# Performance work log

Hardware: AMD Instinct MI355X
Metric: run time of the kernel (lower is better)

The kernel has to match this reference:

```python
import jax, jax.numpy as jnp
import numpy as np

NUM_NEIGHBORS = 10
BN_EPS = 1e-5


def setup_inputs() -> dict:
    key = jax.random.key(0)
    ks = jax.random.split(key, 6)
    B, N, D = 8, 4096, 64
    x = jax.random.normal(ks[0], (B, N, D), jnp.float32)

    def w(k, shape):
        return jax.random.normal(k, shape, jnp.float32) * 0.05

    return {
        "x": x,
        "gamma": jnp.ones((D,), jnp.float32),
        "beta": jnp.zeros((D,), jnp.float32),
        "W1": w(ks[1], (128, 128)), "b1": jnp.zeros((128,), jnp.float32),
        "W2": w(ks[2], (128, 64)), "b2": jnp.zeros((64,), jnp.float32),
        "W3": w(ks[3], (64, 64)), "b3": jnp.zeros((64,), jnp.float32),
        "Wg": w(ks[4], (128, 64)), "bg": jnp.zeros((64,), jnp.float32),
    }


def reference(x, gamma, beta, W1, b1, W2, b2, W3, b3, Wg, bg):
    B, N, D = x.shape
    K = NUM_NEIGHBORS

    # BatchNorm1d in train mode: normalize over all B*N rows with batch stats
    xf = x.reshape(-1, D)
    mu = jnp.mean(xf, axis=0)
    var = jnp.mean((xf - mu) ** 2, axis=0)  # biased, as torch BN uses
    xn = (((xf - mu) / jnp.sqrt(var + BN_EPS)) * gamma + beta).reshape(B, N, D)

    # KNN in feature space (standard DGCNN gather_neighbours)
    sq = jnp.sum(xn * xn, axis=-1)  # [B,N]
    dist = sq[:, :, None] + sq[:, None, :] - 2.0 * jnp.einsum("bnd,bmd->bnm", xn, xn)
    _, idx = jax.lax.top_k(-dist, K)  # [B,N,K] indices of nearest (incl. self)

    # gather neighbor features: neigh[b,n,k,:] = xn[b, idx[b,n,k], :]
    neigh = jax.vmap(lambda f, i: f[i])(xn, idx)  # [B,N,K,D]

    exp = jnp.broadcast_to(xn[:, :, None, :], (B, N, K, D))
    edge = jnp.concatenate([exp, exp - neigh], axis=-1)  # [B,N,K,2D]

    h = jax.nn.relu(edge @ W1 + b1)
    h = jax.nn.relu(h @ W2 + b2)
    h = jax.nn.relu(h @ W3 + b3)  # [B,N,K,64]

    vert = jnp.max(h, axis=2)  # max over neighbors -> [B,N,64]
    g = jnp.max(vert, axis=1, keepdims=True)  # global max-pool [B,1,64]
    cat = jnp.concatenate([vert, jnp.broadcast_to(g, vert.shape)], axis=-1)  # [B,N,128]
    return jax.nn.relu(cat @ Wg + bg)  # [B,N,64]
```

## Files before the change

### kernel.cpp

```cpp
#include <hip/hip_runtime.h>
#include <hip/hip_fp16.h>
#include <float.h>

#define BB 8
#define NN 4096
#define DD 64
#define KNBR 10
#define ROWS (BB*NN)

typedef _Float16 f16x8 __attribute__((ext_vector_type(8)));
typedef float f32x4 __attribute__((ext_vector_type(4)));

__global__ void k_bn_stats(const float* __restrict__ x, float* __restrict__ stats) {
  __shared__ float ls[2][4][64];
  int d = threadIdx.x & 63;
  int g = threadIdx.x >> 6;
  float s = 0.f, s2 = 0.f;
  for (int r = blockIdx.x * 4 + g; r < ROWS; r += gridDim.x * 4) {
    float val = x[r * 64 + d];
    s += val;
    s2 = fmaf(val, val, s2);
  }
  ls[0][g][d] = s;
  ls[1][g][d] = s2;
  __syncthreads();
  if (g == 0) {
    atomicAdd(&stats[d],      ls[0][0][d] + ls[0][1][d] + ls[0][2][d] + ls[0][3][d]);
    atomicAdd(&stats[64 + d], ls[1][0][d] + ls[1][1][d] + ls[1][2][d] + ls[1][3][d]);
  }
}

__global__ void k_bn_finalize(const float* __restrict__ stats,
                              const float* __restrict__ gamma,
                              const float* __restrict__ beta,
                              float* __restrict__ ss) {
  int d = threadIdx.x;
  const float inv = 1.f / 32768.f;
  float mu  = stats[d] * inv;
  float var = stats[64 + d] * inv - mu * mu;
  float sc  = gamma[d] / sqrtf(var + 1e-5f);
  ss[d]      = sc;
  ss[64 + d] = beta[d] - mu * sc;
}

__global__ void k_normalize(const float* __restrict__ x, const float* __restrict__ ss,
                            float* __restrict__ xn, float* __restrict__ sq,
                            _Float16* __restrict__ xh, _Float16* __restrict__ xl) {
  int row = blockIdx.x * 4 + (threadIdx.x >> 6);
  int d = threadIdx.x & 63;
  int idx = row * 64 + d;
  float val = fmaf(x[idx], ss[d], ss[64 + d]);
  xn[idx] = val;
  _Float16 h = (_Float16)val;
  _Float16 l = (_Float16)(val - (float)h);
  xh[idx] = h;
  xl[idx] = l;
  float p = val * val;
  #pragma unroll
  for (int off = 32; off > 0; off >>= 1) p += __shfl_xor(p, off);
  if (d == 0) sq[row] = p;
}

__global__ __launch_bounds__(512, 2) void k_knn(const _Float16* __restrict__ xh,
                                                const _Float16* __restrict__ xl,
                                                const float* __restrict__ sq,
                                                int* __restrict__ knn) {
  __shared__ __align__(16) float Dws[8][2112];
  __shared__ float thrs[64];
  __shared__ int cnts[64];
  const int tid = threadIdx.x;
  const int w = tid >> 6, lane = tid & 63;
  const int l15 = lane & 15, lg = lane >> 4;
  const int b = blockIdx.x >> 6;
  const int rowbase = (blockIdx.x & 63) << 6;
  const int bN = b * NN;
  const _Float16* __restrict__ xhb = xh + (size_t)bN * 64;
  const _Float16* __restrict__ xlb = xl + (size_t)bN * 64;
  const float* __restrict__ sqb = sq + bN;

  f16x8 Ah[4][2], Al[4][2];
  #pragma unroll
  for (int mt = 0; mt < 4; ++mt) {
    #pragma unroll
    for (int ks = 0; ks < 2; ++ks) {
      int r = rowbase + mt * 16 + l15;
      Ah[mt][ks] = *(const f16x8*)(xhb + r * 64 + ks * 32 + lg * 8);
      Al[mt][ks] = *(const f16x8*)(xlb + r * 64 + ks * 32 + lg * 8);
    }
  }

  float bd[10];
  #pragma unroll
  for (int i = 0; i < 10; ++i) bd[i] = FLT_MAX;

  float* Dw = Dws[w];
  float* Drow = Dw + lane * 33;
  const int mbase0 = w * 512;

  #pragma unroll 1
  for (int t = 0; t < 16; ++t) {
    const int mb = mbase0 + t * 32;
    #pragma unroll
    for (int s = 0; s < 2; ++s) {
      const int ms = mb + s * 16;
      f16x8 Bh[2], Bl[2];
      #pragma unroll
      for (int ks = 0; ks < 2; ++ks) {
        Bh[ks] = *(const f16x8*)(xhb + (ms + l15) * 64 + ks * 32 + lg * 8);
        Bl[ks] = *(const f16x8*)(xlb + (ms + l15) * 64 + ks * 32 + lg * 8);
      }
      float sqv = sqb[ms + l15];
      #pragma unroll
      for (int mt = 0; mt < 4; ++mt) {
        f32x4 a = {0.f, 0.f, 0.f, 0.f};
        #pragma unroll
        for (int ks = 0; ks < 2; ++ks) {
          a = __builtin_amdgcn_mfma_f32_16x16x32_f16(Ah[mt][ks], Bh[ks], a, 0, 0, 0);
          a = __builtin_amdgcn_mfma_f32_16x16x32_f16(Ah[mt][ks], Bl[ks], a, 0, 0, 0);
          a = __builtin_amdgcn_mfma_f32_16x16x32_f16(Al[mt][ks], Bh[ks], a, 0, 0, 0);
        }
        int rw = mt * 16 + lg * 4;
        #pragma unroll
        for (int r2 = 0; r2 < 4; ++r2)
          Dw[(rw + r2) * 33 + s * 16 + l15] = fmaf(-2.f, a[r2], sqv);
      }
    }
    #pragma unroll 4
    for (int mm = 0; mm < 32; ++mm) {
      float cd = Drow[mm];
      if (cd < bd[9]) {
        float prev = bd[0];
        bd[0] = fminf(cd, bd[0]);
        #pragma unroll
        for (int j = 1; j < 10; ++j) {
          float cur = bd[j];
          bd[j] = fminf(cur, fmaxf(prev, cd));
          prev = cur;
        }
      }
    }
  }

  __syncthreads();
  float* md = &Dws[0][0];
  #pragma unroll
  for (int i = 0; i < 10; ++i) md[(w * 64 + lane) * 10 + i] = bd[i];
  if (tid < 64) cnts[tid] = 0;
  __syncthreads();
  if (tid < 64) {
    float fd[10];
    #pragma unroll
    for (int i = 0; i < 10; ++i) fd[i] = FLT_MAX;
    for (int li = 0; li < 8; ++li) {
      #pragma unroll 1
      for (int kk = 0; kk < 10; ++kk) {
        float cd = md[(li * 64 + tid) * 10 + kk];
        if (cd < fd[9]) {
          float prev = fd[0];
          fd[0] = fminf(cd, fd[0]);
          #pragma unroll
          for (int j = 1; j < 10; ++j) {
            float cur = fd[j];
            fd[j] = fminf(cur, fmaxf(prev, cd));
            prev = cur;
          }
        } else break;
      }
    }
    thrs[tid] = fd[9];
  }
  __syncthreads();

  float thv[4][4];
  #pragma unroll
  for (int mt = 0; mt < 4; ++mt)
    #pragma unroll
    for (int r2 = 0; r2 < 4; ++r2)
      thv[mt][r2] = thrs[mt * 16 + lg * 4 + r2];
  int* knnrow = knn + (size_t)(bN + rowbase) * KNBR;

  #pragma unroll 1
  for (int t = 0; t < 16; ++t) {
    const int mb = mbase0 + t * 32;
    #pragma unroll
    for (int s = 0; s < 2; ++s) {
      const int ms = mb + s * 16;
      f16x8 Bh[2], Bl[2];
      #pragma unroll
      for (int ks = 0; ks < 2; ++ks) {
        Bh[ks] = *(const f16x8*)(xhb + (ms + l15) * 64 + ks * 32 + lg * 8);
        Bl[ks] = *(const f16x8*)(xlb + (ms + l15) * 64 + ks * 32 + lg * 8);
      }
      float sqv = sqb[ms + l15];
      #pragma unroll
      for (int mt = 0; mt < 4; ++mt) {
        f32x4 a = {0.f, 0.f, 0.f, 0.f};
        #pragma unroll
        for (int ks = 0; ks < 2; ++ks) {
          a = __builtin_amdgcn_mfma_f32_16x16x32_f16(Ah[mt][ks], Bh[ks], a, 0, 0, 0);
          a = __builtin_amdgcn_mfma_f32_16x16x32_f16(Ah[mt][ks], Bl[ks], a, 0, 0, 0);
          a = __builtin_amdgcn_mfma_f32_16x16x32_f16(Al[mt][ks], Bh[ks], a, 0, 0, 0);
        }
        #pragma unroll
        for (int r2 = 0; r2 < 4; ++r2) {
          float cd = fmaf(-2.f, a[r2], sqv);
          if (cd <= thv[mt][r2]) {
            int row = mt * 16 + lg * 4 + r2;
            int slot = atomicAdd(&cnts[row], 1);
            if (slot < KNBR) knnrow[row * KNBR + slot] = bN + ms + l15;
          }
        }
      }
    }
  }
}

__global__ void k_uv(const float* __restrict__ xn, const float* __restrict__ W1,
                     const float* __restrict__ b1, float* __restrict__ u,
                     float* __restrict__ v) {
  __shared__ float xs[64 * 64];
  const int tid = threadIdx.x;
  const int o = tid & 127;
  const bool isU = tid < 128;
  const int rowbase = blockIdx.x * 64;

  float wreg[64];
  #pragma unroll
  for (int d = 0; d < 64; ++d) {
    float bw = W1[(64 + d) * 128 + o];
    wreg[d] = isU ? (W1[d * 128 + o] + bw) : bw;
  }
  const float bb = isU ? b1[o] : 0.f;
  float* __restrict__ dst = isU ? u : v;

  {
    const float4* s4 = (const float4*)(xn + rowbase * 64);
    float4* d4 = (float4*)xs;
    #pragma unroll
    for (int i = 0; i < 4; ++i) d4[tid + 256 * i] = s4[tid + 256 * i];
  }
  __syncthreads();

  for (int r = 0; r < 64; ++r) {
    const float4* xr = (const float4*)(xs + r * 64);
    float a0 = bb, a1 = 0.f, a2 = 0.f, a3 = 0.f;
    #pragma unroll
    for (int q = 0; q < 16; ++q) {
      float4 xv = xr[q];
      a0 = fmaf(xv.x, wreg[4 * q + 0], a0);
      a1 = fmaf(xv.y, wreg[4 * q + 1], a1);
      a2 = fmaf(xv.z, wreg[4 * q + 2], a2);
      a3 = fmaf(xv.w, wreg[4 * q + 3], a3);
    }
    dst[(rowbase + r) * 128 + o] = (a0 + a1) + (a2 + a3);
  }
}

__global__ __launch_bounds__(256, 2) void k_edge(const float* __restrict__ uu,
                                                 const float* __restrict__ vv,
                                                 const int* __restrict__ knn,
                                                 const float* __restrict__ W2,
                                                 const float* __restrict__ b2,
                                                 const float* __restrict__ W3,
                                                 const float* __restrict__ b3,
                                                 float* __restrict__ vert) {
  __shared__ __align__(16) _Float16 W3Ts[64 * 72];
  __shared__ __align__(16) _Float16 h2buf[4][16 * 88];
  __shared__ int vmaxs[4][512];
  const int tid = threadIdx.x;
  const int w = tid >> 6, lane = tid & 63;
  const int l15 = lane & 15, lg = lane >> 4;

  for (int i = tid; i < 64 * 64; i += 256) {
    int o3 = i >> 6, k2 = i & 63;
    W3Ts[o3 * 72 + k2] = (_Float16)W3[k2 * 64 + o3];
  }
  f16x8 w2f[4][4];
  #pragma unroll
  for (int ks = 0; ks < 4; ++ks) {
    #pragma unroll
    for (int nt = 0; nt < 4; ++nt) {
      f16x8 t;
      #pragma unroll
      for (int j = 0; j < 8; ++j)
        t[j] = (_Float16)W2[(ks * 32 + lg * 8 + j) * 64 + nt * 16 + l15];
      w2f[ks][nt] = t;
    }
  }
  float bias2[4], bias3[4];
  #pragma unroll
  for (int nt = 0; nt < 4; ++nt) { bias2[nt] = b2[nt * 16 + l15]; bias3[nt] = b3[nt * 16 + l15]; }

  _Float16* h2w = h2buf[w];
  int* vmaxw = vmaxs[w];
  #pragma unroll
  for (int q = 0; q < 8; ++q) vmaxw[lane * 8 + q] = 0;
  __syncthreads();

  const int g = blockIdx.x * 4 + w;
  const int n0 = g * 8;
  const int ebase = n0 * KNBR;
  #pragma unroll 1
  for (int mt = 0; mt < 5; ++mt) {
    const int e = mt * 16 + l15;
    const int m = knn[ebase + e];
    const int n = n0 + e / 10;
    const float* Up = uu + (size_t)n * 128 + lg * 8;
    const float* Vp = vv + (size_t)m * 128 + lg * 8;
    f16x8 A[4];
    #pragma unroll
    for (int ks = 0; ks < 4; ++ks) {
      float4 ua = *(const float4*)(Up + ks * 32);
      float4 ub = *(const float4*)(Up + ks * 32 + 4);
      float4 va = *(const float4*)(Vp + ks * 32);
      float4 vb = *(const float4*)(Vp + ks * 32 + 4);
      f16x8 t;
      t[0] = (_Float16)fmaxf(ua.x - va.x, 0.f);
      t[1] = (_Float16)fmaxf(ua.y - va.y, 0.f);
      t[2] = (_Float16)fmaxf(ua.z - va.z, 0.f);
      t[3] = (_Float16)fmaxf(ua.w - va.w, 0.f);
      t[4] = (_Float16)fmaxf(ub.x - vb.x, 0.f);
      t[5] = (_Float16)fmaxf(ub.y - vb.y, 0.f);
      t[6] = (_Float16)fmaxf(ub.z - vb.z, 0.f);
      t[7] = (_Float16)fmaxf(ub.w - vb.w, 0.f);
      A[ks] = t;
    }
    f32x4 acc[4];
    #pragma unroll
    for (int nt = 0; nt < 4; ++nt) { float bbv = bias2[nt]; acc[nt] = (f32x4){bbv, bbv, bbv, bbv}; }
    #pragma unroll
    for (int ks = 0; ks < 4; ++ks) {
      #pragma unroll
      for (int nt = 0; nt < 4; ++nt)
        acc[nt] = __builtin_amdgcn_mfma_f32_16x16x32_f16(A[ks], w2f[ks][nt], acc[nt], 0, 0, 0);
    }
    #pragma unroll
    for (int nt = 0; nt < 4; ++nt) {
      #pragma unroll
      for (int r = 0; r < 4; ++r)
        h2w[(lg * 4 + r) * 88 + nt * 16 + l15] = (_Float16)fmaxf(acc[nt][r], 0.f);
    }
    f16x8 A3[2];
    #pragma unroll
    for (int ks2 = 0; ks2 < 2; ++ks2)
      A3[ks2] = *(const f16x8*)(h2w + l15 * 88 + ks2 * 32 + lg * 8);
    f32x4 c3[4];
    #pragma unroll
    for (int nt = 0; nt < 4; ++nt) { float bbv = bias3[nt]; c3[nt] = (f32x4){bbv, bbv, bbv, bbv}; }
    #pragma unroll
    for (int ks2 = 0; ks2 < 2; ++ks2) {
      #pragma unroll
      for (int nt = 0; nt < 4; ++nt) {
        f16x8 bf = *(const f16x8*)(W3Ts + (nt * 16 + l15) * 72 + ks2 * 32 + lg * 8);
        c3[nt] = __builtin_amdgcn_mfma_f32_16x16x32_f16(A3[ks2], bf, c3[nt], 0, 0, 0);
      }
    }
    #pragma unroll
    for (int nt = 0; nt < 4; ++nt) {
      #pragma unroll
      for (int r = 0; r < 4; ++r) {
        float val = fmaxf(c3[nt][r], 0.f);
        int e2 = mt * 16 + lg * 4 + r;
        int p = e2 / 10;
        atomicMax(&vmaxw[p * 64 + nt * 16 + l15], __float_as_int(val));
      }
    }
  }
  {
    int p2 = lane >> 3, c0 = (lane & 7) * 8;
    const int* vp = &vmaxw[p2 * 64 + c0];
    float4 r0, r1;
    r0.x = __int_as_float(vp[0]); r0.y = __int_as_float(vp[1]);
    r0.z = __int_as_float(vp[2]); r0.w = __int_as_float(vp[3]);
    r1.x = __int_as_float(vp[4]); r1.y = __int_as_float(vp[5]);
    r1.z = __int_as_float(vp[6]); r1.w = __int_as_float(vp[7]);
    *(float4*)(vert + (size_t)(n0 + p2) * 64 + c0) = r0;
    *(float4*)(vert + (size_t)(n0 + p2) * 64 + c0 + 4) = r1;
  }
}

__global__ void k_gmax(const float* __restrict__ vert, float* __restrict__ g) {
  __shared__ float red[4][64];
  int b = blockIdx.x >> 4, chunk = blockIdx.x & 15;
  int sub = threadIdx.x >> 6, o = threadIdx.x & 63;
  float vm = 0.f;
  for (int j = 0; j < 64; ++j) {
    int r = chunk * 256 + j * 4 + sub;
    vm = fmaxf(vm, vert[(b * NN + r) * 64 + o]);
  }
  red[sub][o] = vm;
  __syncthreads();
  if (sub == 0) {
    float mm = fmaxf(fmaxf(red[0][o], red[1][o]), fmaxf(red[2][o], red[3][o]));
    atomicMax((int*)&g[b * 64 + o], __float_as_int(mm));
  }
}

__global__ void k_gb(const float* __restrict__ g, const float* __restrict__ Wg,
                     const float* __restrict__ bg, float* __restrict__ gb) {
  int t = threadIdx.x;
  int b = t >> 6, o = t & 63;
  float acc = bg[o];
  #pragma unroll
  for (int i = 0; i < 64; ++i)
    acc = fmaf(g[b * 64 + i], Wg[(64 + i) * 64 + o], acc);
  gb[b * 64 + o] = acc;
}

__global__ void k_final(const float* __restrict__ vert, const float* __restrict__ Wg,
                        const float* __restrict__ gb, float* __restrict__ out) {
  __shared__ float Wgs[64 * 64];
  int tid = threadIdx.x, w = tid >> 6, lane = tid & 63;
  for (int i = tid; i < 4096; i += 256) Wgs[i] = Wg[i];
  __syncthreads();
  int gw = blockIdx.x * 4 + w;
  for (int j = 0; j < 4; ++j) {
    int n = gw + 8192 * j;
    int b = n >> 12;
    float vrow = vert[n * 64 + lane];
    float ac0 = gb[b * 64 + lane], ac1 = 0.f, ac2 = 0.f, ac3 = 0.f;
    #pragma unroll
    for (int i = 0; i < 64; i += 4) {
      ac0 = fmaf(__shfl(vrow, i),     Wgs[i * 64 + lane],       ac0);
      ac1 = fmaf(__shfl(vrow, i + 1), Wgs[(i + 1) * 64 + lane], ac1);
      ac2 = fmaf(__shfl(vrow, i + 2), Wgs[(i + 2) * 64 + lane], ac2);
      ac3 = fmaf(__shfl(vrow, i + 3), Wgs[(i + 3) * 64 + lane], ac3);
    }
    out[n * 64 + lane] = fmaxf((ac0 + ac1) + (ac2 + ac3), 0.f);
  }
}

extern "C" void kernel_launch(void* const* d_in, const int* in_sizes, int n_in,
                              void* d_out, int out_size, void* d_ws, size_t ws_size,
                              hipStream_t stream) {
  const float* x     = (const float*)d_in[0];
  const float* gamma = (const float*)d_in[1];
  const float* beta  = (const float*)d_in[2];
  const float* W1    = (const float*)d_in[3];
  const float* b1    = (const float*)d_in[4];
  const float* W2    = (const float*)d_in[5];
  const float* b2    = (const float*)d_in[6];
  const float* W3    = (const float*)d_in[7];
  const float* b3    = (const float*)d_in[8];
  const float* Wg    = (const float*)d_in[9];
  const float* bg    = (const float*)d_in[10];
  float* out = (float*)d_out;

  float* ws    = (float*)d_ws;
  float* stats = ws;
  float* ss    = ws + 128;
  float* xn    = ws + 256;
  float* sq    = xn + 2097152;
  int*   knn   = (int*)(sq + 32768);
  float* u     = (float*)(knn + 327680);
  float* v     = u + 4194304;
  float* vert  = v + 4194304;
  float* g     = vert + 2097152;
  float* gb    = g + 512;
  _Float16* xh = (_Float16*)(gb + 512);
  _Float16* xl = (_Float16*)(gb + 512 + 1048576);

  hipMemsetAsync(stats, 0, 128 * sizeof(float), stream);
  hipMemsetAsync(g, 0, 512 * sizeof(float), stream);

  k_bn_stats<<<256, 256, 0, stream>>>(x, stats);
  k_bn_finalize<<<1, 64, 0, stream>>>(stats, gamma, beta, ss);
  k_normalize<<<8192, 256, 0, stream>>>(x, ss, xn, sq, xh, xl);
  k_knn<<<512, 512, 0, stream>>>(xh, xl, sq, knn);
  k_uv<<<512, 256, 0, stream>>>(xn, W1, b1, u, v);
  k_edge<<<1024, 256, 0, stream>>>(u, v, knn, W2, b2, W3, b3, vert);
  k_gmax<<<128, 256, 0, stream>>>(vert, g);
  k_gb<<<1, 512, 0, stream>>>(g, Wg, bg, gb);
  k_final<<<2048, 256, 0, stream>>>(vert, Wg, gb, out);
}
```

Before: 523.1 us.

## Split KNN candidate range across two blocks, stage B tiles in swizzled LDS

The KNN kernel is split so that each query tile is handled by two 256-thread blocks, each scanning half of the candidate points. Each half writes its 10 best (distance, index) pairs, and a new selection kernel merges the 20 candidates per row into the final top-10. Candidate tiles are now prefetched into registers and staged through XOR-swizzled LDS rather than loaded directly from global memory per MFMA. The intent is more blocks and better load latency hiding, at the cost of an extra launch, a scratch buffer aliased onto u, and a second pass over the candidate distances.

```diff
diff --git a/kernel.cpp b/kernel.cpp
--- a/kernel.cpp
+++ b/kernel.cpp
@@ -61,22 +61,30 @@
   if (d == 0) sq[row] = p;
 }
 
-__global__ __launch_bounds__(512, 2) void k_knn(const _Float16* __restrict__ xh,
-                                                const _Float16* __restrict__ xl,
-                                                const float* __restrict__ sq,
-                                                int* __restrict__ knn) {
-  __shared__ __align__(16) float Dws[8][2112];
+__global__ __launch_bounds__(256, 2) void k_knn_ab(const _Float16* __restrict__ xh,
+                                                   const _Float16* __restrict__ xl,
+                                                   const float* __restrict__ sq,
+                                                   float* __restrict__ pairs,
+                                                   int* __restrict__ pidx) {
+  __shared__ __align__(16) char lds[33792];
   __shared__ float thrs[64];
   __shared__ int cnts[64];
   const int tid = threadIdx.x;
   const int w = tid >> 6, lane = tid & 63;
   const int l15 = lane & 15, lg = lane >> 4;
-  const int b = blockIdx.x >> 6;
-  const int rowbase = (blockIdx.x & 63) << 6;
+  const int bid = blockIdx.x;
+  const int h = bid & 1;
+  const int qb = bid >> 1;
+  const int b = qb >> 6;
+  const int rowbase = (qb & 63) << 6;
   const int bN = b * NN;
   const _Float16* __restrict__ xhb = xh + (size_t)bN * 64;
   const _Float16* __restrict__ xlb = xl + (size_t)bN * 64;
-  const float* __restrict__ sqb = sq + bN;
+
+  char* wbase = lds + w * 8448;
+  char* Bhi = wbase;
+  char* Blo = wbase + 2048;
+  float* Dw = (float*)(wbase + 4096);
 
   f16x8 Ah[4][2], Al[4][2];
   #pragma unroll
@@ -93,40 +101,59 @@
   #pragma unroll
   for (int i = 0; i < 10; ++i) bd[i] = FLT_MAX;
 
-  float* Dw = Dws[w];
-  float* Drow = Dw + lane * 33;
-  const int mbase0 = w * 512;
+  int srow[2], scc[2];
+  #pragma unroll
+  for (int i = 0; i < 2; ++i) { int c = i * 64 + lane; srow[i] = c >> 3; scc[i] = c & 7; }
+
+  const int mbase0 = h * 2048 + w * 512;
+  f16x8 sh[2], sl[2];
+  #pragma unroll
+  for (int i = 0; i < 2; ++i) {
+    sh[i] = *(const f16x8*)(xhb + (mbase0 + srow[i]) * 64 + scc[i] * 8);
+    sl[i] = *(const f16x8*)(xlb + (mbase0 + srow[i]) * 64 + scc[i] * 8);
+  }
+
+  float* Drow = Dw + lane * 17;
 
   #pragma unroll 1
-  for (int t = 0; t < 16; ++t) {
-    const int mb = mbase0 + t * 32;
-    #pragma unroll
-    for (int s = 0; s < 2; ++s) {
-      const int ms = mb + s * 16;
-      f16x8 Bh[2], Bl[2];
+  for (int t = 0; t < 32; ++t) {
+    const int mb = mbase0 + t * 16;
+    const int mb2 = (t < 31) ? mb + 16 : mb;
+    float sqv = sq[bN + mb + l15];
+    #pragma unroll
+    for (int i = 0; i < 2; ++i) {
+      int off = srow[i] * 128 + 16 * (scc[i] ^ (srow[i] & 7));
+      *(f16x8*)(Bhi + off) = sh[i];
+      *(f16x8*)(Blo + off) = sl[i];
+    }
+    #pragma unroll
+    for (int i = 0; i < 2; ++i) {
+      sh[i] = *(const f16x8*)(xhb + (mb2 + srow[i]) * 64 + scc[i] * 8);
+      sl[i] = *(const f16x8*)(xlb + (mb2 + srow[i]) * 64 + scc[i] * 8);
+    }
+    f16x8 Bh[2], Bl[2];
+    #pragma unroll
+    for (int ks = 0; ks < 2; ++ks) {
+      int off = l15 * 128 + 16 * ((ks * 4 + lg) ^ (l15 & 7));
+      Bh[ks] = *(const f16x8*)(Bhi + off);
+      Bl[ks] = *(const f16x8*)(Blo + off);
+    }
+    #pragma unroll
+    for (int mt = 0; mt < 4; ++mt) {
+      f32x4 a0 = {0.f, 0.f, 0.f, 0.f};
       #pragma unroll
       for (int ks = 0; ks < 2; ++ks) {
-        Bh[ks] = *(const f16x8*)(xhb + (ms + l15) * 64 + ks * 32 + lg * 8);
-        Bl[ks] = *(const f16x8*)(xlb + (ms + l15) * 64 + ks * 32 + lg * 8);
-      }
-      float sqv = sqb[ms + l15];
-      #pragma unroll
-      for (int mt = 0; mt < 4; ++mt) {
-        f32x4 a = {0.f, 0.f, 0.f, 0.f};
-        #pragma unroll
-        for (int ks = 0; ks < 2; ++ks) {
-          a = __builtin_amdgcn_mfma_f32_16x16x32_f16(Ah[mt][ks], Bh[ks], a, 0, 0, 0);
-          a = __builtin_amdgcn_mfma_f32_16x16x32_f16(Ah[mt][ks], Bl[ks], a, 0, 0, 0);
-          a = __builtin_amdgcn_mfma_f32_16x16x32_f16(Al[mt][ks], Bh[ks], a, 0, 0, 0);
-        }
-        int rw = mt * 16 + lg * 4;
-        #pragma unroll
-        for (int r2 = 0; r2 < 4; ++r2)
-          Dw[(rw + r2) * 33 + s * 16 + l15] = fmaf(-2.f, a[r2], sqv);
-      }
+        a0 = __builtin_amdgcn_mfma_f32_16x16x32_f16(Ah[mt][ks], Bh[ks], a0, 0, 0, 0);
+        a0 = __builtin_amdgcn_mfma_f32_16x16x32_f16(Ah[mt][ks], Bl[ks], a0, 0, 0, 0);
+        a0 = __builtin_amdgcn_mfma_f32_16x16x32_f16(Al[mt][ks], Bh[ks], a0, 0, 0, 0);
+      }
+      int rw = mt * 16 + lg * 4;
+      #pragma unroll
+      for (int r2 = 0; r2 < 4; ++r2)
+        Dw[(rw + r2) * 17 + l15] = fmaf(-2.f, a0[r2], sqv);
     }
     #pragma unroll 4
-    for (int mm = 0; mm < 32; ++mm) {
+    for (int mm = 0; mm < 16; ++mm) {
       float cd = Drow[mm];
       if (cd < bd[9]) {
         float prev = bd[0];
@@ -142,7 +169,7 @@
   }
 
   __syncthreads();
-  float* md = &Dws[0][0];
+  float* md = (float*)lds;
   #pragma unroll
   for (int i = 0; i < 10; ++i) md[(w * 64 + lane) * 10 + i] = bd[i];
   if (tid < 64) cnts[tid] = 0;
@@ -151,10 +178,10 @@
     float fd[10];
     #pragma unroll
     for (int i = 0; i < 10; ++i) fd[i] = FLT_MAX;
-    for (int li = 0; li < 8; ++li) {
+    for (int w2 = 0; w2 < 4; ++w2) {
       #pragma unroll 1
       for (int kk = 0; kk < 10; ++kk) {
-        float cd = md[(li * 64 + tid) * 10 + kk];
+        float cd = md[(w2 * 64 + tid) * 10 + kk];
         if (cd < fd[9]) {
           float prev = fd[0];
           fd[0] = fminf(cd, fd[0]);
@@ -177,42 +204,86 @@
     #pragma unroll
     for (int r2 = 0; r2 < 4; ++r2)
       thv[mt][r2] = thrs[mt * 16 + lg * 4 + r2];
-  int* knnrow = knn + (size_t)(bN + rowbase) * KNBR;
-
+
+  float* prow = pairs + (size_t)(bN + rowbase) * 20 + h * 10;
+  int*   irow = pidx  + (size_t)(bN + rowbase) * 20 + h * 10;
+
+  #pragma unroll
+  for (int i = 0; i < 2; ++i) {
+    sh[i] = *(const f16x8*)(xhb + (mbase0 + srow[i]) * 64 + scc[i] * 8);
+    sl[i] = *(const f16x8*)(xlb + (mbase0 + srow[i]) * 64 + scc[i] * 8);
+  }
   #pragma unroll 1
-  for (int t = 0; t < 16; ++t) {
-    const int mb = mbase0 + t * 32;
-    #pragma unroll
-    for (int s = 0; s < 2; ++s) {
-      const int ms = mb + s * 16;
-      f16x8 Bh[2], Bl[2];
+  for (int t = 0; t < 32; ++t) {
+    const int mb = mbase0 + t * 16;
+    const int mb2 = (t < 31) ? mb + 16 : mb;
+    float sqv = sq[bN + mb + l15];
+    #pragma unroll
+    for (int i = 0; i < 2; ++i) {
+      int off = srow[i] * 128 + 16 * (scc[i] ^ (srow[i] & 7));
+      *(f16x8*)(Bhi + off) = sh[i];
+      *(f16x8*)(Blo + off) = sl[i];
+    }
+    #pragma unroll
+    for (int i = 0; i < 2; ++i) {
+      sh[i] = *(const f16x8*)(xhb + (mb2 + srow[i]) * 64 + scc[i] * 8);
+      sl[i] = *(const f16x8*)(xlb + (mb2 + srow[i]) * 64 + scc[i] * 8);
+    }
+    f16x8 Bh[2], Bl[2];
+    #pragma unroll
+    for (int ks = 0; ks < 2; ++ks) {
+      int off = l15 * 128 + 16 * ((ks * 4 + lg) ^ (l15 & 7));
+      Bh[ks] = *(const f16x8*)(Bhi + off);
+      Bl[ks] = *(const f16x8*)(Blo + off);
+    }
+    #pragma unroll
+    for (int mt = 0; mt < 4; ++mt) {
+      f32x4 a0 = {0.f, 0.f, 0.f, 0.f};
       #pragma unroll
       for (int ks = 0; ks < 2; ++ks) {
-        Bh[ks] = *(const f16x8*)(xhb + (ms + l15) * 64 + ks * 32 + lg * 8);
-        Bl[ks] = *(const f16x8*)(xlb + (ms + l15) * 64 + ks * 32 + lg * 8);
-      }
-      float sqv = sqb[ms + l15];
-      #pragma unroll
-      for (int mt = 0; mt < 4; ++mt) {
-        f32x4 a = {0.f, 0.f, 0.f, 0.f};
-        #pragma unroll
-        for (int ks = 0; ks < 2; ++ks) {
-          a = __builtin_amdgcn_mfma_f32_16x16x32_f16(Ah[mt][ks], Bh[ks], a, 0, 0, 0);
-          a = __builtin_amdgcn_mfma_f32_16x16x32_f16(Ah[mt][ks], Bl[ks], a, 0, 0, 0);
-          a = __builtin_amdgcn_mfma_f32_16x16x32_f16(Al[mt][ks], Bh[ks], a, 0, 0, 0);
-        }
-        #pragma unroll
-        for (int r2 = 0; r2 < 4; ++r2) {
-          float cd = fmaf(-2.f, a[r2], sqv);
-          if (cd <= thv[mt][r2]) {
-            int row = mt * 16 + lg * 4 + r2;
-            int slot = atomicAdd(&cnts[row], 1);
-            if (slot < KNBR) knnrow[row * KNBR + slot] = bN + ms + l15;
+        a0 = __builtin_amdgcn_mfma_f32_16x16x32_f16(Ah[mt][ks], Bh[ks], a0, 0, 0, 0);
+        a0 = __builtin_amdgcn_mfma_f32_16x16x32_f16(Ah[mt][ks], Bl[ks], a0, 0, 0, 0);
+        a0 = __builtin_amdgcn_mfma_f32_16x16x32_f16(Al[mt][ks], Bh[ks], a0, 0, 0, 0);
+      }
+      #pragma unroll
+      for (int r2 = 0; r2 < 4; ++r2) {
+        float d0 = fmaf(-2.f, a0[r2], sqv);
+        int row = mt * 16 + lg * 4 + r2;
+        if (d0 <= thv[mt][r2]) {
+          int slot = atomicAdd(&cnts[row], 1);
+          if (slot < KNBR) {
+            prow[row * 20 + slot] = d0;
+            irow[row * 20 + slot] = bN + mb + l15;
           }
         }
       }
     }
   }
+}
+
+__global__ void k_sel(const float* __restrict__ pairs, const int* __restrict__ pidx,
+                      int* __restrict__ knn) {
+  int gid = blockIdx.x * 256 + threadIdx.x;
+  const float* pd = pairs + (size_t)gid * 20;
+  const int*   pi = pidx  + (size_t)gid * 20;
+  float fd[10]; int fi[10];
+  #pragma unroll
+  for (int i = 0; i < 10; ++i) { fd[i] = FLT_MAX; fi[i] = 0; }
+  #pragma unroll 1
+  for (int k = 0; k < 20; ++k) {
+    float cd = pd[k]; int ci = pi[k];
+    if (cd < fd[9]) {
+      #pragma unroll
+      for (int j = 0; j < 10; ++j) {
+        bool swp = cd < fd[j];
+        float tf = fd[j]; int ti = fi[j];
+        fd[j] = swp ? cd : tf; fi[j] = swp ? ci : ti;
+        cd = swp ? tf : cd;    ci = swp ? ti : ci;
+      }
+    }
+  }
+  #pragma unroll
+  for (int k = 0; k < 10; ++k) knn[(size_t)gid * KNBR + k] = fi[k];
 }
 
 __global__ void k_uv(const float* __restrict__ xn, const float* __restrict__ W1,
@@ -460,13 +531,17 @@
   _Float16* xh = (_Float16*)(gb + 512);
   _Float16* xl = (_Float16*)(gb + 512 + 1048576);
 
+  float* pairs = u;
+  int*   pidx  = (int*)(u + 655360);
+
   hipMemsetAsync(stats, 0, 128 * sizeof(float), stream);
   hipMemsetAsync(g, 0, 512 * sizeof(float), stream);
 
   k_bn_stats<<<256, 256, 0, stream>>>(x, stats);
   k_bn_finalize<<<1, 64, 0, stream>>>(stats, gamma, beta, ss);
   k_normalize<<<8192, 256, 0, stream>>>(x, ss, xn, sq, xh, xl);
-  k_knn<<<512, 512, 0, stream>>>(xh, xl, sq, knn);
+  k_knn_ab<<<1024, 256, 0, stream>>>(xh, xl, sq, pairs, pidx);
+  k_sel<<<128, 256, 0, stream>>>(pairs, pidx, knn);
   k_uv<<<512, 256, 0, stream>>>(xn, W1, b1, u, v);
   k_edge<<<1024, 256, 0, stream>>>(u, v, knn, W2, b2, W3, b3, vert);
   k_gmax<<<128, 256, 0, stream>>>(vert, g);
```

After: 482.0 us. -7.9%, faster.
